# Kernel optimization log

Measured on AMD Instinct MI355X. Metric: run time of the kernel, lower is better.

## Reference

```python
import jax, jax.numpy as jnp
import numpy as np

MUL0, MUL1 = 32, 16          # multiplicities of 0e and 1o irreps
DIM = MUL0 + 3 * MUL1        # flat irrep feature dim = 80
N = 1_000_000                # number of nodes
INV_SQRT3 = float(1.0 / np.sqrt(3.0))  # CG coeff for 1o x 1o -> 0e (dot product)


def setup_inputs() -> dict:
    key = jax.random.key(0)
    ks = jax.random.split(key, 10)
    f = lambda k, s: jax.random.normal(k, s, dtype=jnp.float32)
    return {
        "node_feats": f(ks[0], (N, DIM)),
        "node_messages": f(ks[1], (N, DIM)),
        "W00_1": f(ks[2], (MUL0, MUL0, MUL0)),
        "W01_1": f(ks[3], (MUL0, MUL1, MUL1)),
        "W11_1": f(ks[4], (MUL1, MUL1, MUL0)),
        "W00_2": f(ks[5], (MUL0, MUL0, MUL0)),
        "W01_2": f(ks[6], (MUL0, MUL1, MUL1)),
        "W11_2": f(ks[7], (MUL1, MUL1, MUL0)),
        "L0": f(ks[8], (MUL0, MUL0)),
        "L1": f(ks[9], (MUL1, MUL1)),
    }


def _split(x):
    # x: [N, 80] -> scalars [N, 32], vectors [N, 16, 3]
    return x[:, :MUL0], x[:, MUL0:].reshape(-1, MUL1, 3)


def _tensor_square(x, W00, W01, W11):
    """Weighted symmetric tensor square of x with itself (e3nn o3.TensorSquare).
    Paths: 0e*0e->0e, 1o*1o->0e (CG = dot/sqrt(3)), 0e*1o->1o.
    Each uvw path carries a 1/sqrt(fan_in) normalization."""
    x0, x1 = _split(x)
    out0 = jnp.einsum('nu,nv,uvw->nw', x0, x0, W00) / float(MUL0)
    out0 = out0 + jnp.einsum('nui,nvi,uvw->nw', x1, x1, W11) * (INV_SQRT3 / float(MUL1))
    out1 = jnp.einsum('nu,nvi,uvw->nwi', x0, x1, W01) / float(np.sqrt(MUL0 * MUL1))
    return out0, out1  # [N, MUL0], [N, MUL1, 3]


def reference(node_feats, node_messages, W00_1, W01_1, W11_1,
              W00_2, W01_2, W11_2, L0, L1):
    a0, a1 = _tensor_square(node_feats, W00_1, W01_1, W11_1)
    b0, b1 = _tensor_square(node_messages, W00_2, W01_2, W11_2)
    y0, y1 = a0 + b0, a1 + b1
    # equivariant Linear: per-l channel mixing with 1/sqrt(fan_in)
    z0 = (y0 @ L0) / float(np.sqrt(MUL0))
    z1 = jnp.einsum('nwi,wv->nvi', y1, L1) / float(np.sqrt(MUL1))
    return jnp.concatenate([z0, z1.reshape(-1, 3 * MUL1)], axis=1)  # [N, 80]
```

## Files before the change

### kernel.cpp

```cpp
#include <hip/hip_runtime.h>
#include <hip/hip_bf16.h>


typedef __attribute__((ext_vector_type(8)))  _Float16 half8;
typedef __attribute__((ext_vector_type(2)))  _Float16 h16x2;
typedef __attribute__((ext_vector_type(16))) float    f32x16;
typedef __attribute__((ext_vector_type(4)))  float    f32x4;
typedef __attribute__((ext_vector_type(4)))  int      iv4;

#define V00_LDS_BYTES 82944
#define XBUF_BYTES    11264
#define SMEM_BYTES    (V00_LDS_BYTES + 7 * XBUF_BYTES)
#define WS_V11_BYTE   82944
#define WS_V01_BYTE   107520
#define WAVE_STRIDE   1792

__device__ __forceinline__ void gll16(const void* g, void* l)
{
    __builtin_amdgcn_global_load_lds(
        (const __attribute__((address_space(1))) void*)g,
        (__attribute__((address_space(3))) void*)l,
        16, 0, 0);
}

#define WAIT_VM0()   asm volatile("s_waitcnt vmcnt(0)" ::: "memory")
#define WAIT_LGKM0() asm volatile("s_waitcnt lgkmcnt(0)" ::: "memory")
#define SCHED_FENCE() __builtin_amdgcn_sched_barrier(0)

__device__ __forceinline__ unsigned pkrtz(float a, float b)
{
    auto h = __builtin_amdgcn_cvt_pkrtz(a, b);
    unsigned u;
    __builtin_memcpy(&u, &h, 4);
    return u;
}
__device__ __forceinline__ unsigned pkmul(unsigned a, unsigned b)
{
    h16x2 r = __builtin_bit_cast(h16x2, a) * __builtin_bit_cast(h16x2, b);
    return __builtin_bit_cast(unsigned, r);
}
__device__ __forceinline__ unsigned pkfma(unsigned a, unsigned b, unsigned c)
{
    h16x2 r = __builtin_bit_cast(h16x2, a) * __builtin_bit_cast(h16x2, b)
            + __builtin_bit_cast(h16x2, c);
    return __builtin_bit_cast(unsigned, r);
}
__device__ __forceinline__ unsigned splat_sel(unsigned pair, int h1)
{
    unsigned v = h1 ? (pair >> 16) : (pair & 0xffffu);
    return v | (v << 16);
}
__device__ __forceinline__ float lo_f(unsigned p)
{
    return (float)__builtin_bit_cast(h16x2, p)[0];
}
__device__ __forceinline__ float hi_f(unsigned p)
{
    return (float)__builtin_bit_cast(h16x2, p)[1];
}

__device__ __forceinline__ f32x16 mfma_f16(iv4 a, iv4 b, f32x16 c)
{
    return __builtin_amdgcn_mfma_f32_32x32x16_f16(
        __builtin_bit_cast(half8, a), __builtin_bit_cast(half8, b), c, 0, 0, 0);
}

__device__ __forceinline__ void dec00(int kk, int& r, int& u0)
{
    if      (kk < 4)  { r = 0; u0 = kk * 2; }
    else if (kk < 12) { r = 1; u0 = (kk - 4) * 2; }
    else if (kk < 24) { r = 2; u0 = (kk - 12) * 2; }
    else              { r = 3; u0 = (kk - 24) * 2; }
}
__device__ __forceinline__ void dec11(int kk, int& r, int& u0)
{
    if (kk < 4) { r = 0; u0 = kk * 2; }
    else        { r = 1; u0 = (kk - 4) * 2; }
}

__global__ void prep_weights(const float* __restrict__ W00_1, const float* __restrict__ W01_1,
                             const float* __restrict__ W11_1, const float* __restrict__ W00_2,
                             const float* __restrict__ W01_2, const float* __restrict__ W11_2,
                             const float* __restrict__ L0,    const float* __restrict__ L1,
                             _Float16* __restrict__ ws)
{
    int t = blockIdx.x * 256 + threadIdx.x;
    const float s00 = 1.0f / (32.0f * sqrtf(32.0f));
    const float s11 = 0.57735026919f / (16.0f * sqrtf(32.0f));
    const float s01 = 1.0f / sqrtf(8192.0f);

    if (t < 2 * 32 * 648) {
        int k  = t % 648;
        int rw = t / 648;
        int wp = rw & 31, s = rw >> 5;
        const float* W = s ? W00_2 : W00_1;
        float val = 0.f;
        int kk = k >> 4;
        if (kk < 40) {
            int h = (k >> 3) & 1, j = k & 7, r, u0;
            dec00(kk, r, u0);
            int u = u0 + h, v = 8 * r + j;
            if (v >= u) {
                float acc = 0.f;
                for (int w = 0; w < 32; ++w) {
                    float c = W[(u * 32 + v) * 32 + w];
                    if (u != v) c += W[(v * 32 + u) * 32 + w];
                    acc += c * L0[w * 32 + wp];
                }
                val = acc * s00;
            }
        }
        ws[t] = (_Float16)val;
        return;
    }
    t -= 2 * 32 * 648;
    if (t < 2 * 32 * 192) {
        int k  = t % 192;
        int rw = t / 192;
        int wp = rw & 31, s = rw >> 5;
        const float* W = s ? W11_2 : W11_1;
        int kk = k >> 4, h = (k >> 3) & 1, j = k & 7, r, u0;
        dec11(kk, r, u0);
        int u = u0 + h, v = 8 * r + j;
        float val = 0.f;
        if (v >= u) {
            float acc = 0.f;
            for (int w = 0; w < 32; ++w) {
                float c = W[(u * 16 + v) * 32 + w];
                if (u != v) c += W[(v * 16 + u) * 32 + w];
                acc += c * L0[w * 32 + wp];
            }
            val = acc * s11;
        }
        ws[2 * 32 * 648 + t] = (_Float16)val;
        return;
    }
    t -= 2 * 32 * 192;
    if (t < 2 * 256 * 32) {
        int u  = t & 31;
        int rw = t >> 5;
        int row = rw & 255, s = rw >> 8;
        int v = row >> 4, wp = row & 15;
        const float* W = s ? W01_2 : W01_1;
        float acc = 0.f;
        for (int w = 0; w < 16; ++w)
            acc += W[(u * 16 + v) * 16 + w] * L1[w * 16 + wp];
        ws[2 * 32 * 648 + 2 * 32 * 192 + t] = (_Float16)(acc * s01);
    }
}

__device__ __forceinline__ void stage32(const float* __restrict__ src, char* xbuf, int lane)
{
#pragma unroll
    for (int st = 0; st < 11; ++st) {
        int q  = st * 64 + lane;
        int r  = q / 21;
        int cc = q - r * 21;
        if (r > 31) { r = 31; cc = 20; }
        int col = cc * 4;
        if (col > 76) col = 76;
        gll16(src + r * 80 + col, xbuf + st * 1024);
    }
}

__global__ __launch_bounds__(448)
void tsq_main(const float* __restrict__ xf, const float* __restrict__ xm,
              const unsigned short* __restrict__ wsb, float* __restrict__ out,
              int ntiles)
{
    __shared__ __align__(16) char smem[SMEM_BYTES];
    const int lane = threadIdx.x & 63;
    const int wid  = (int)(threadIdx.x >> 6);
    const int h1   = lane >> 5;
    const int wp   = lane & 31;
    char* xbuf = smem + V00_LDS_BYTES + wid * XBUF_BYTES;

    for (int c = wid; c < 81; c += 7)
        gll16((const char*)wsb + c * 1024 + lane * 16, smem + c * 1024);
    WAIT_VM0();
    __syncthreads();

    const int wg = blockIdx.x * 7 + wid;
    if (wg < ntiles)
        stage32(xf + (size_t)wg * 2560, xbuf, lane);

    for (int t = wg; t < ntiles; t += WAVE_STRIDE) {
        const int tn = t + WAVE_STRIDE;

        f32x16 acc0;
#pragma unroll
        for (int e = 0; e < 16; ++e) acc0[e] = 0.f;
        float z1a[8][3];
#pragma unroll
        for (int d = 0; d < 8; ++d) { z1a[d][0] = 0.f; z1a[d][1] = 0.f; z1a[d][2] = 0.f; }

#pragma unroll 1
        for (int s = 0; s < 2; ++s) {
            WAIT_VM0();

            unsigned xh0[16], xh1[3][8];
            const char* myrow = xbuf + wp * 336;
#pragma unroll
            for (int g = 0; g < 2; ++g) {
#pragma unroll
                for (int k = 4 * g; k < 4 * g + 4; ++k) {
                    float4 v = *reinterpret_cast<const float4*>(myrow + k * 16);
                    xh0[2 * k + 0] = pkrtz(v.x, v.y);
                    xh0[2 * k + 1] = pkrtz(v.z, v.w);
                }
                SCHED_FENCE();
            }
#pragma unroll
            for (int pp = 0; pp < 4; ++pp) {
                float4 a = *reinterpret_cast<const float4*>(myrow + 128 + pp * 48);
                float4 b = *reinterpret_cast<const float4*>(myrow + 128 + pp * 48 + 16);
                float4 c = *reinterpret_cast<const float4*>(myrow + 128 + pp * 48 + 32);
                xh1[0][2 * pp + 0] = pkrtz(a.x, a.w);
                xh1[1][2 * pp + 0] = pkrtz(a.y, b.x);
                xh1[2][2 * pp + 0] = pkrtz(a.z, b.y);
                xh1[0][2 * pp + 1] = pkrtz(b.z, c.y);
                xh1[1][2 * pp + 1] = pkrtz(b.w, c.z);
                xh1[2][2 * pp + 1] = pkrtz(c.x, c.w);
                SCHED_FENCE();
            }
            WAIT_LGKM0();

            if (s == 0)            stage32(xm + (size_t)t  * 2560, xbuf, lane);
            else if (tn < ntiles)  stage32(xf + (size_t)tn * 2560, xbuf, lane);
            SCHED_FENCE();

            const char* v00b = smem + s * 41472 + wp * 1296 + h1 * 16;
#pragma unroll
            for (int kk = 0; kk < 40; ++kk) {
                int rr, u0; dec00(kk, rr, u0);
                unsigned ub = splat_sel(xh0[u0 >> 1], h1);
                iv4 bf;
#pragma unroll
                for (int q = 0; q < 4; ++q)
                    bf[q] = (int)pkmul(ub, xh0[4 * rr + q]);
                iv4 af = *reinterpret_cast<const iv4*>(v00b + kk * 32);
                acc0 = mfma_f16(af, bf, acc0);
                if (kk & 1) SCHED_FENCE();
            }

            const char* v11g = (const char*)wsb + WS_V11_BYTE
                             + (size_t)((s * 32 + wp) * 192) * 2 + h1 * 16;
#pragma unroll
            for (int kk = 0; kk < 12; ++kk) {
                int rr, u0; dec11(kk, rr, u0);
                int q0 = u0 >> 1;
                unsigned b0 = splat_sel(xh1[0][q0], h1);
                unsigned b1 = splat_sel(xh1[1][q0], h1);
                unsigned b2 = splat_sel(xh1[2][q0], h1);
                iv4 bf;
#pragma unroll
                for (int q = 0; q < 4; ++q) {
                    int vp = 4 * rr + q;
                    unsigned d = pkmul(b0, xh1[0][vp]);
                    d = pkfma(b1, xh1[1][vp], d);
                    d = pkfma(b2, xh1[2][vp], d);
                    bf[q] = (int)d;
                }
                iv4 af = *reinterpret_cast<const iv4*>(v11g + kk * 32);
                acc0 = mfma_f16(af, bf, acc0);
                if (kk & 1) SCHED_FENCE();
            }

            iv4 b01[2];
#pragma unroll
            for (int kk = 0; kk < 2; ++kk)
#pragma unroll
                for (int q = 0; q < 4; ++q)
                    b01[kk][q] = (int)xh0[kk * 8 + 4 * h1 + q];

            const char* v01g = (const char*)wsb + WS_V01_BYTE
                             + (size_t)((s * 256 + wp) * 32) * 2 + h1 * 16;
#pragma unroll
            for (int m = 0; m < 8; ++m) {
                iv4 a0 = *reinterpret_cast<const iv4*>(v01g + m * 2048);
                iv4 a1 = *reinterpret_cast<const iv4*>(v01g + m * 2048 + 32);
                f32x16 tq;
#pragma unroll
                for (int e = 0; e < 16; ++e) tq[e] = 0.f;
                tq = mfma_f16(a0, b01[0], tq);
                tq = mfma_f16(a1, b01[1], tq);
                float x1f[2][3];
#pragma unroll
                for (int i = 0; i < 3; ++i) {
                    unsigned p = xh1[i][m];
                    x1f[0][i] = lo_f(p);
                    x1f[1][i] = hi_f(p);
                }
#pragma unroll
                for (int reg = 0; reg < 16; ++reg) {
                    int vloc = reg >> 3;
                    int d    = (reg & 3) + 4 * ((reg >> 2) & 1);
                    z1a[d][0] = fmaf(tq[reg], x1f[vloc][0], z1a[d][0]);
                    z1a[d][1] = fmaf(tq[reg], x1f[vloc][1], z1a[d][1]);
                    z1a[d][2] = fmaf(tq[reg], x1f[vloc][2], z1a[d][2]);
                }
                SCHED_FENCE();
            }
        }

        float* orow = out + (size_t)(t * 32 + wp) * 80;
#pragma unroll
        for (int qn = 0; qn < 4; ++qn) {
            f32x4 vz = { acc0[4 * qn + 0], acc0[4 * qn + 1],
                         acc0[4 * qn + 2], acc0[4 * qn + 3] };
            *reinterpret_cast<f32x4*>(orow + 8 * qn + 4 * h1) = vz;
        }
        float* p1 = orow + 32 + 12 * h1;
        {
            f32x4 a = { z1a[0][0], z1a[0][1], z1a[0][2], z1a[1][0] };
            f32x4 b = { z1a[1][1], z1a[1][2], z1a[2][0], z1a[2][1] };
            f32x4 c = { z1a[2][2], z1a[3][0], z1a[3][1], z1a[3][2] };
            *reinterpret_cast<f32x4*>(p1 + 0) = a;
            *reinterpret_cast<f32x4*>(p1 + 4) = b;
            *reinterpret_cast<f32x4*>(p1 + 8) = c;
        }
        float* p2 = orow + 56 + 12 * h1;
        {
            f32x4 a = { z1a[4][0], z1a[4][1], z1a[4][2], z1a[5][0] };
            f32x4 b = { z1a[5][1], z1a[5][2], z1a[6][0], z1a[6][1] };
            f32x4 c = { z1a[6][2], z1a[7][0], z1a[7][1], z1a[7][2] };
            *reinterpret_cast<f32x4*>(p2 + 0) = a;
            *reinterpret_cast<f32x4*>(p2 + 4) = b;
            *reinterpret_cast<f32x4*>(p2 + 8) = c;
        }
    }
}

extern "C" void kernel_launch(void* const* d_in, const int* in_sizes, int n_in,
                              void* d_out, int out_size, void* d_ws, size_t ws_size,
                              hipStream_t stream)
{
    const float* xf    = (const float*)d_in[0];
    const float* xm    = (const float*)d_in[1];
    const float* W00_1 = (const float*)d_in[2];
    const float* W01_1 = (const float*)d_in[3];
    const float* W11_1 = (const float*)d_in[4];
    const float* W00_2 = (const float*)d_in[5];
    const float* W01_2 = (const float*)d_in[6];
    const float* W11_2 = (const float*)d_in[7];
    const float* L0    = (const float*)d_in[8];
    const float* L1    = (const float*)d_in[9];

    const int N      = in_sizes[0] / 80;
    const int ntiles = N / 32;

    prep_weights<<<274, 256, 0, stream>>>(W00_1, W01_1, W11_1,
                                          W00_2, W01_2, W11_2,
                                          L0, L1, (_Float16*)d_ws);

    tsq_main<<<256, 448, 0, stream>>>(xf, xm,
                                      (const unsigned short*)d_ws,
                                      (float*)d_out, ntiles);
}
```

Measured before the change: 448.7 us.

## Move W00 tail weights from LDS to global to fit eight waves per block

The folded W00 weight table is split so that only the first 24 k-steps stay in LDS, while the last 16 k-steps are read directly from global memory (L2/L1 cached) through a new workspace region. The freed LDS lets each block hold eight per-wave staging buffers instead of seven, so the block size goes from 448 to 512 threads and the tile stride is raised to match. This trades extra global-memory weight loads in the inner MFMA loop for more waves per CU to hide input-streaming latency.

```diff
diff --git a/kernel.cpp b/kernel.cpp
--- a/kernel.cpp
+++ b/kernel.cpp
@@ -8,12 +8,13 @@
 typedef __attribute__((ext_vector_type(4)))  float    f32x4;
 typedef __attribute__((ext_vector_type(4)))  int      iv4;
 
-#define V00_LDS_BYTES 82944
+#define V00_LDS_BYTES 50176
 #define XBUF_BYTES    11264
-#define SMEM_BYTES    (V00_LDS_BYTES + 7 * XBUF_BYTES)
+#define SMEM_BYTES    (V00_LDS_BYTES + 8 * XBUF_BYTES)
+#define WS_TAIL_BYTE  50176
 #define WS_V11_BYTE   82944
 #define WS_V01_BYTE   107520
-#define WAVE_STRIDE   1792
+#define WAVE_STRIDE   2048
 
 __device__ __forceinline__ void gll16(const void* g, void* l)
 {
@@ -76,6 +77,18 @@
 {
     if (kk < 4) { r = 0; u0 = kk * 2; }
     else        { r = 1; u0 = (kk - 4) * 2; }
+}
+
+__device__ __forceinline__ float fold00(const float* W, const float* L0,
+                                        int u, int v, int wp)
+{
+    float acc = 0.f;
+    for (int w = 0; w < 32; ++w) {
+        float c = W[(u * 32 + v) * 32 + w];
+        if (u != v) c += W[(v * 32 + u) * 32 + w];
+        acc += c * L0[w * 32 + wp];
+    }
+    return acc * (1.0f / (32.0f * 5.65685424949f));
 }
 
 __global__ void prep_weights(const float* __restrict__ W00_1, const float* __restrict__ W01_1,
@@ -85,35 +98,39 @@
                              _Float16* __restrict__ ws)
 {
     int t = blockIdx.x * 256 + threadIdx.x;
-    const float s00 = 1.0f / (32.0f * sqrtf(32.0f));
-    const float s11 = 0.57735026919f / (16.0f * sqrtf(32.0f));
+    const float s11 = 0.57735026919f / (16.0f * 5.65685424949f);
     const float s01 = 1.0f / sqrtf(8192.0f);
 
-    if (t < 2 * 32 * 648) {
-        int k  = t % 648;
-        int rw = t / 648;
+    if (t < 2 * 32 * 392) {
+        int k  = t % 392;
+        int rw = t / 392;
         int wp = rw & 31, s = rw >> 5;
         const float* W = s ? W00_2 : W00_1;
         float val = 0.f;
         int kk = k >> 4;
-        if (kk < 40) {
+        if (k < 384) {
             int h = (k >> 3) & 1, j = k & 7, r, u0;
             dec00(kk, r, u0);
             int u = u0 + h, v = 8 * r + j;
-            if (v >= u) {
-                float acc = 0.f;
-                for (int w = 0; w < 32; ++w) {
-                    float c = W[(u * 32 + v) * 32 + w];
-                    if (u != v) c += W[(v * 32 + u) * 32 + w];
-                    acc += c * L0[w * 32 + wp];
-                }
-                val = acc * s00;
-            }
+            if (v >= u) val = fold00(W, L0, u, v, wp);
         }
         ws[t] = (_Float16)val;
         return;
     }
-    t -= 2 * 32 * 648;
+    t -= 2 * 32 * 392;
+    if (t < 2 * 32 * 256) {
+        int k  = t % 256;
+        int rw = t / 256;
+        int wp = rw & 31, s = rw >> 5;
+        const float* W = s ? W00_2 : W00_1;
+        int kk = 24 + (k >> 4), h = (k >> 3) & 1, j = k & 7, r, u0;
+        dec00(kk, r, u0);
+        int u = u0 + h, v = 8 * r + j;
+        float val = (v >= u) ? fold00(W, L0, u, v, wp) : 0.f;
+        ws[2 * 32 * 392 + t] = (_Float16)val;
+        return;
+    }
+    t -= 2 * 32 * 256;
     if (t < 2 * 32 * 192) {
         int k  = t % 192;
         int rw = t / 192;
@@ -163,7 +180,7 @@
     }
 }
 
-__global__ __launch_bounds__(448)
+__global__ __launch_bounds__(512)
 void tsq_main(const float* __restrict__ xf, const float* __restrict__ xm,
               const unsigned short* __restrict__ wsb, float* __restrict__ out,
               int ntiles)
@@ -175,12 +192,12 @@
     const int wp   = lane & 31;
     char* xbuf = smem + V00_LDS_BYTES + wid * XBUF_BYTES;
 
-    for (int c = wid; c < 81; c += 7)
+    for (int c = wid; c < 49; c += 8)
         gll16((const char*)wsb + c * 1024 + lane * 16, smem + c * 1024);
     WAIT_VM0();
     __syncthreads();
 
-    const int wg = blockIdx.x * 7 + wid;
+    const int wg = blockIdx.x * 8 + wid;
     if (wg < ntiles)
         stage32(xf + (size_t)wg * 2560, xbuf, lane);
 
@@ -229,9 +246,9 @@
             else if (tn < ntiles)  stage32(xf + (size_t)tn * 2560, xbuf, lane);
             SCHED_FENCE();
 
-            const char* v00b = smem + s * 41472 + wp * 1296 + h1 * 16;
-#pragma unroll
-            for (int kk = 0; kk < 40; ++kk) {
+            const char* v00b = smem + s * 25088 + wp * 784 + h1 * 16;
+#pragma unroll
+            for (int kk = 0; kk < 24; ++kk) {
                 int rr, u0; dec00(kk, rr, u0);
                 unsigned ub = splat_sel(xh0[u0 >> 1], h1);
                 iv4 bf;
@@ -239,6 +256,21 @@
                 for (int q = 0; q < 4; ++q)
                     bf[q] = (int)pkmul(ub, xh0[4 * rr + q]);
                 iv4 af = *reinterpret_cast<const iv4*>(v00b + kk * 32);
+                acc0 = mfma_f16(af, bf, acc0);
+                if (kk & 1) SCHED_FENCE();
+            }
+
+            const char* v00t = (const char*)wsb + WS_TAIL_BYTE
+                             + (size_t)((s * 32 + wp) * 512) + h1 * 16;
+#pragma unroll
+            for (int kk = 24; kk < 40; ++kk) {
+                int rr, u0; dec00(kk, rr, u0);
+                unsigned ub = splat_sel(xh0[u0 >> 1], h1);
+                iv4 bf;
+#pragma unroll
+                for (int q = 0; q < 4; ++q)
+                    bf[q] = (int)pkmul(ub, xh0[4 * rr + q]);
+                iv4 af = *reinterpret_cast<const iv4*>(v00t + (kk - 24) * 32);
                 acc0 = mfma_f16(af, bf, acc0);
                 if (kk & 1) SCHED_FENCE();
             }
@@ -353,7 +385,7 @@
                                           W00_2, W01_2, W11_2,
                                           L0, L1, (_Float16*)d_ws);
 
-    tsq_main<<<256, 448, 0, stream>>>(xf, xm,
+    tsq_main<<<256, 512, 0, stream>>>(xf, xm,
                                       (const unsigned short*)d_ws,
                                       (float*)d_out, ntiles);
 }
```

Measured after the change: 510.3 us. 13.7% more time.
